# Performance work log

Hardware: AMD Instinct MI355X
Metric: run time of the kernel (lower is better)

## Reference

```python
import jax, jax.numpy as jnp
import numpy as np

B, T, D, E, H = 4, 2048, 1024, 4, 8
EPS = 1e-5


def _uniform(k, shape, bound):
    return jax.random.uniform(k, shape, jnp.float32, -bound, bound)


def setup_inputs() -> dict:
    key = jax.random.key(0)
    ks = jax.random.split(key, 12)
    wb = np.sqrt(6.0 / D) / np.sqrt(6.0)  # kaiming_uniform(a=sqrt5) bound ~ 1/sqrt(D)... keep simple
    wb = 1.0 / np.sqrt(D)
    return {
        "x": jax.random.normal(ks[0], (B, T, D), jnp.float32),
        "router_prob": jax.random.uniform(ks[1], (B, T, E), jnp.float32),
        "norm_w": jnp.ones((D,), jnp.float32),
        "norm_b": jnp.zeros((D,), jnp.float32),
        "q_w": _uniform(ks[2], (D, D), wb),
        "q_b": _uniform(ks[3], (D,), wb),
        "k_w": _uniform(ks[4], (D, D), wb),
        "k_b": _uniform(ks[5], (D,), wb),
        "v_w": _uniform(ks[6], (D, D), wb),
        "v_b": _uniform(ks[7], (D,), wb),
        "o_w": _uniform(ks[8], (D, D), wb),
        "o_b": _uniform(ks[9], (D,), wb),
    }


def _layernorm(x, w, b):
    mu = jnp.mean(x, axis=-1, keepdims=True)
    var = jnp.mean(jnp.square(x - mu), axis=-1, keepdims=True)
    return (x - mu) * jax.lax.rsqrt(var + EPS) * w + b


def reference(x, router_prob, norm_w, norm_b, q_w, q_b, k_w, k_b, v_w, v_b, o_w, o_b):
    e_cnt = router_prob.shape[2]
    b, t, d = x.shape
    n = t // e_cnt
    h = H
    scale = d ** (-0.5)  # note: original uses model_dim**-0.5, not head_dim

    qs, ks_, vs = [], [], []
    for e in range(e_cnt):
        xe = x[:, e * n:(e + 1) * n, :]
        xn = _layernorm(xe, norm_w, norm_b)
        m = d // (2 ** e)
        xm = xn[..., :m]  # [b, n, m] matryoshka slice
        # F.linear(xm, W[:, :m], bias): out = xm @ W[:, :m]^T + b -> [b, n, d]
        qs.append(jnp.einsum('bnm,dm->bnd', xm, q_w[:, :m]) + q_b)
        ks_.append(jnp.einsum('bnm,dm->bnd', xm, k_w[:, :m]) + k_b)
        vs.append(jnp.einsum('bnm,dm->bnd', xm, v_w[:, :m]) + v_b)
    q = jnp.concatenate(qs, axis=1)
    k = jnp.concatenate(ks_, axis=1)
    v = jnp.concatenate(vs, axis=1)

    dh = d // h
    q = q.reshape(b, t, h, dh).transpose(0, 2, 1, 3)  # b h t dh
    k = k.reshape(b, t, h, dh).transpose(0, 2, 1, 3)
    v = v.reshape(b, t, h, dh).transpose(0, 2, 1, 3)

    attn = jnp.einsum('bhqd,bhkd->bhqk', q, k) * scale
    attn = jax.nn.softmax(attn, axis=-1)  # dropout = identity in eval
    attn_out = jnp.einsum('bhqk,bhkd->bhqd', attn, v)
    attn_out = attn_out.transpose(0, 2, 1, 3).reshape(b, t, d)

    outs = []
    for e in range(e_cnt):
        sl = slice(e * n, (e + 1) * n)
        m = d // (2 ** e)
        xm = attn_out[:, sl, :m]
        out = jnp.einsum('bnm,om->bno', xm, o_w[:m, :m]) + o_b[:m]  # [b, n, m]
        pad = d - m
        if pad:
            out = jnp.pad(out, ((0, 0), (0, 0), (0, pad)))
        outs.append(out + x[:, sl, :])
    return jnp.concatenate(outs, axis=1)
```

## Files before the change

kernel.cpp:

```cpp
#include <hip/hip_runtime.h>
#include <hip/hip_bf16.h>

#define DEV static __device__ __forceinline__

typedef __attribute__((ext_vector_type(4))) float f32x4;
typedef __attribute__((ext_vector_type(8))) short s16x8;
typedef __attribute__((ext_vector_type(4))) unsigned int u32x4;

constexpr int Bn = 4, Tn = 2048, Dn = 1024, Hn = 8, DH = 128;
constexpr float EPSF = 1e-5f;
constexpr float QSCALE = 0.0450842200277801f;

DEV unsigned short f2bf(float f) {
    unsigned int u = __float_as_uint(f);
    u += 0x7FFF + ((u >> 16) & 1);
    return (unsigned short)(u >> 16);
}

DEV f32x4 mfma16(s16x8 a, s16x8 b, f32x4 c) {
    return __builtin_amdgcn_mfma_f32_16x16x32_bf16(a, b, c, 0, 0, 0);
}

DEV float ex2(float x) {
    float r;
    asm("v_exp_f32 %0, %1" : "=v"(r) : "v"(x));
    return r;
}

DEV unsigned int cvtpk(float lo, float hi) {
    unsigned int r;
    asm("v_cvt_pk_bf16_f32 %0, %1, %2" : "=v"(r) : "v"(lo), "v"(hi));
    return r;
}

typedef __attribute__((address_space(1))) const unsigned int GU32;
typedef __attribute__((address_space(3))) unsigned int LU32;
DEV void gload16(const void* g, void* l) {
    __builtin_amdgcn_global_load_lds((GU32*)g, (LU32*)l, 16, 0, 0);
}

__global__ void cvt_w_kernel(const float* __restrict__ qw, const float* __restrict__ kw,
                             const float* __restrict__ vw, const float* __restrict__ ow,
                             unsigned short* __restrict__ dst) {
    int idx = blockIdx.x * blockDim.x + threadIdx.x;
    const int total = 4 * Dn * Dn;
    for (; idx < total; idx += gridDim.x * blockDim.x) {
        int sel = idx >> 20;
        int off = idx & (Dn * Dn - 1);
        const float* src = sel == 0 ? qw : sel == 1 ? kw : sel == 2 ? vw : ow;
        dst[idx] = f2bf(src[off]);
    }
}

__global__ __launch_bounds__(256) void ln_kernel(const float* __restrict__ x,
                                                 const float* __restrict__ w,
                                                 const float* __restrict__ b,
                                                 unsigned short* __restrict__ xn) {
    int tok = blockIdx.x;
    int tid = threadIdx.x;
    const float* xp = x + (size_t)tok * Dn;
    float4 v = ((const float4*)xp)[tid];
    float s = v.x + v.y + v.z + v.w;
    float q = v.x * v.x + v.y * v.y + v.z * v.z + v.w * v.w;
    for (int off = 32; off; off >>= 1) {
        s += __shfl_xor(s, off);
        q += __shfl_xor(q, off);
    }
    __shared__ float red[8];
    __shared__ float stats[2];
    int wid = tid >> 6, lane = tid & 63;
    if (lane == 0) { red[wid] = s; red[4 + wid] = q; }
    __syncthreads();
    if (tid == 0) {
        float ts = red[0] + red[1] + red[2] + red[3];
        float tq = red[4] + red[5] + red[6] + red[7];
        float mu = ts / Dn;
        float var = tq / Dn - mu * mu;
        stats[0] = mu;
        stats[1] = rsqrtf(var + EPSF);
    }
    __syncthreads();
    float mu = stats[0], rs = stats[1];
    int c = tid * 4;
    ushort4 o;
    o.x = f2bf((v.x - mu) * rs * w[c + 0] + b[c + 0]);
    o.y = f2bf((v.y - mu) * rs * w[c + 1] + b[c + 1]);
    o.z = f2bf((v.z - mu) * rs * w[c + 2] + b[c + 2]);
    o.w = f2bf((v.w - mu) * rs * w[c + 3] + b[c + 3]);
    ((ushort4*)(xn + (size_t)tok * Dn))[tid] = o;
}

__global__ __launch_bounds__(256) void qkv_gemm(const unsigned short* __restrict__ xn,
                                                const unsigned short* __restrict__ wmat,
                                                const float* __restrict__ qb_,
                                                const float* __restrict__ kb_,
                                                const float* __restrict__ vb_,
                                                unsigned short* __restrict__ outq,
                                                unsigned short* __restrict__ outk,
                                                unsigned short* __restrict__ vt) {
    int rowbase = blockIdx.x * 128;
    int colbase = blockIdx.y * 128;
    int matid = blockIdx.z;
    const unsigned short* W = wmat + (size_t)matid * Dn * Dn;
    const float* bias = matid == 0 ? qb_ : matid == 1 ? kb_ : vb_;
    float oscale = matid == 0 ? QSCALE : 1.0f;
    int e = (rowbase & (Tn - 1)) >> 9;
    int m = Dn >> e;

    __shared__ alignas(16) unsigned short At[2][128 * 32];
    __shared__ alignas(16) unsigned short Bt[2][128 * 32];

    int tid = threadIdx.x;
    int lane = tid & 63, wv = tid >> 6;
    int wr = (wv >> 1) * 64, wc = (wv & 1) * 64;
    int fr = lane & 15, fg = lane >> 4;
    int srow = tid >> 2, scol = (tid & 3) * 8;
    const unsigned short* ga0 = xn + (size_t)(rowbase + srow) * Dn + scol;
    const unsigned short* ga1 = xn + (size_t)(rowbase + 64 + srow) * Dn + scol;
    const unsigned short* gb0 = W + (size_t)(colbase + srow) * Dn + scol;
    const unsigned short* gb1 = W + (size_t)(colbase + 64 + srow) * Dn + scol;

    f32x4 acc[4][4] = {};

    gload16(ga0, &At[0][tid * 8]);
    gload16(ga1, &At[0][2048 + tid * 8]);
    gload16(gb0, &Bt[0][tid * 8]);
    gload16(gb1, &Bt[0][2048 + tid * 8]);
    __syncthreads();

    for (int k = 0; k < m; k += 32) {
        int cur = (k >> 5) & 1;
        if (k + 32 < m) {
            int nb = cur ^ 1, kn = k + 32;
            gload16(ga0 + kn, &At[nb][tid * 8]);
            gload16(ga1 + kn, &At[nb][2048 + tid * 8]);
            gload16(gb0 + kn, &Bt[nb][tid * 8]);
            gload16(gb1 + kn, &Bt[nb][2048 + tid * 8]);
        }
        s16x8 a[4], b[4];
        #pragma unroll
        for (int i = 0; i < 4; i++) a[i] = *(const s16x8*)&At[cur][(wr + i * 16 + fr) * 32 + fg * 8];
        #pragma unroll
        for (int j = 0; j < 4; j++) b[j] = *(const s16x8*)&Bt[cur][(wc + j * 16 + fr) * 32 + fg * 8];
        #pragma unroll
        for (int i = 0; i < 4; i++)
            #pragma unroll
            for (int j = 0; j < 4; j++) acc[i][j] = mfma16(a[i], b[j], acc[i][j]);
        __syncthreads();
    }

    if (matid == 2) {
        #pragma unroll
        for (int i = 0; i < 4; i++)
            #pragma unroll
            for (int j = 0; j < 4; j++) {
                int col = colbase + wc + j * 16 + fr;
                float bv = bias[col];
                int row0 = rowbase + wr + i * 16 + fg * 4;
                int bb = row0 >> 11, tl = row0 & (Tn - 1);
                int w32 = tl & 31;
                int tlp = (tl & ~31) | (((w32 >> 2) & 3) * 8 + ((w32 >> 4) & 1) * 4);
                size_t base = (((size_t)bb * Hn + (col >> 7)) * DH + (col & (DH - 1))) * Tn + tlp;
                ushort4 o;
                o.x = f2bf(acc[i][j][0] + bv);
                o.y = f2bf(acc[i][j][1] + bv);
                o.z = f2bf(acc[i][j][2] + bv);
                o.w = f2bf(acc[i][j][3] + bv);
                *(ushort4*)&vt[base] = o;
            }
    } else {
        unsigned short* out = matid == 0 ? outq : outk;
        #pragma unroll
        for (int i = 0; i < 4; i++)
            #pragma unroll
            for (int j = 0; j < 4; j++) {
                int col = colbase + wc + j * 16 + fr;
                float bv = bias[col];
                #pragma unroll
                for (int r = 0; r < 4; r++) {
                    int row = rowbase + wr + i * 16 + fg * 4 + r;
                    out[(size_t)row * Dn + col] = f2bf((acc[i][j][r] + bv) * oscale);
                }
            }
    }
}

__global__ __launch_bounds__(256, 2) void attn_kernel(const unsigned short* __restrict__ Q,
                                                      const unsigned short* __restrict__ K,
                                                      const unsigned short* __restrict__ VT,
                                                      unsigned short* __restrict__ AO) {
    int f = blockIdx.x;
    int qi = f >> 5;
    int bh = f & 31;
    int b = bh >> 3, h = bh & 7;
    int qbase = qi * 128;
    int tid = threadIdx.x;
    int wv = tid >> 6, lane = tid & 63;
    int fr = lane & 15, fg = lane >> 4;

    __shared__ alignas(16) unsigned short Kt[2][64 * 128];
    __shared__ alignas(16) unsigned short Vt[2][128 * 64];

    s16x8 bq[2][4];
    #pragma unroll
    for (int hh = 0; hh < 2; hh++) {
        const size_t qr = ((size_t)b * Tn + qbase + wv * 32 + hh * 16 + fr) * Dn + h * DH;
        #pragma unroll
        for (int c = 0; c < 4; c++) bq[hh][c] = *(const s16x8*)&Q[qr + c * 32 + fg * 8];
    }

    f32x4 acc[2][8] = {};
    float m_run[2] = {-1e30f, -1e30f};
    float l_run[2] = {0.f, 0.f};

    const unsigned short* Kbase = K + (size_t)b * Tn * Dn + h * DH;
    const unsigned short* Vbase = VT + ((size_t)b * Hn + h) * DH * Tn;

    int k_row_lo = tid >> 4, k_chk = tid & 15;
    int v_row_lo = tid >> 3, v_chk = tid & 7;

    auto STAGE = [&](int t, int buf) {
        int kb = t * 64;
        #pragma unroll
        for (int p = 0; p < 4; p++) {
            int row = p * 16 + k_row_lo;
            int chunk = k_chk ^ (row & 7);
            gload16(Kbase + (size_t)(kb + row) * Dn + chunk * 8,
                    &Kt[buf][p * 2048 + tid * 8]);
        }
        #pragma unroll
        for (int p = 0; p < 4; p++) {
            int row = p * 32 + v_row_lo;
            int chunk = v_chk ^ (row & 7);
            gload16(Vbase + (size_t)row * Tn + kb + chunk * 8,
                    &Vt[buf][p * 2048 + tid * 8]);
        }
    };

    STAGE(0, 0);
    __syncthreads();

    for (int t = 0; t < Tn / 64; t++) {
        int cur = t & 1;
        if (t < Tn / 64 - 1) STAGE(t + 1, cur ^ 1);

        const unsigned short* KtC = &Kt[cur][0];
        const unsigned short* VtC = &Vt[cur][0];

        f32x4 s[2][4] = {};
        #pragma unroll
        for (int c = 0; c < 4; c++) {
            #pragma unroll
            for (int kt = 0; kt < 4; kt++) {
                s16x8 ak = *(const s16x8*)&KtC[(kt * 16 + fr) * 128 +
                                               (((c * 4 + fg) ^ (fr & 7)) * 8)];
                s[0][kt] = mfma16(ak, bq[0][c], s[0][kt]);
                s[1][kt] = mfma16(ak, bq[1][c], s[1][kt]);
            }
        }

        float mx[2];
        #pragma unroll
        for (int hh = 0; hh < 2; hh++) {
            float v = s[hh][0][0];
            #pragma unroll
            for (int kt = 0; kt < 4; kt++)
                #pragma unroll
                for (int r = 0; r < 4; r++) v = fmaxf(v, s[hh][kt][r]);
            v = fmaxf(v, __shfl_xor(v, 16));
            v = fmaxf(v, __shfl_xor(v, 32));
            mx[hh] = v;
        }

        if (!__all(mx[0] - m_run[0] <= 8.0f && mx[1] - m_run[1] <= 8.0f)) {
            #pragma unroll
            for (int hh = 0; hh < 2; hh++) {
                float mnew = fmaxf(m_run[hh], mx[hh]);
                float fsc = ex2(m_run[hh] - mnew);
                l_run[hh] *= fsc;
                float fw[4];
                #pragma unroll
                for (int r = 0; r < 4; r++) fw[r] = __shfl(fsc, fg * 4 + r);
                #pragma unroll
                for (int n = 0; n < 8; n++)
                    #pragma unroll
                    for (int r = 0; r < 4; r++) acc[hh][n][r] *= fw[r];
                m_run[hh] = mnew;
            }
        }

        s16x8 pa[2][2];
        #pragma unroll
        for (int hh = 0; hh < 2; hh++) {
            float p[16];
            float sum = 0.f;
            #pragma unroll
            for (int kt = 0; kt < 4; kt++)
                #pragma unroll
                for (int r = 0; r < 4; r++) {
                    float ev = ex2(s[hh][kt][r] - m_run[hh]);
                    p[kt * 4 + r] = ev;
                    sum += ev;
                }
            sum += __shfl_xor(sum, 16);
            sum += __shfl_xor(sum, 32);
            l_run[hh] += sum;
            #pragma unroll
            for (int ks = 0; ks < 2; ks++) {
                u32x4 pw;
                pw.x = cvtpk(p[ks * 8 + 0], p[ks * 8 + 1]);
                pw.y = cvtpk(p[ks * 8 + 2], p[ks * 8 + 3]);
                pw.z = cvtpk(p[ks * 8 + 4], p[ks * 8 + 5]);
                pw.w = cvtpk(p[ks * 8 + 6], p[ks * 8 + 7]);
                pa[hh][ks] = __builtin_bit_cast(s16x8, pw);
            }
        }

        #pragma unroll
        for (int ks = 0; ks < 2; ks++) {
            #pragma unroll
            for (int n = 0; n < 8; n++) {
                int row = n * 16 + fr;
                s16x8 bv = *(const s16x8*)&VtC[row * 64 +
                                               (((ks * 4 + fg) ^ (fr & 7)) * 8)];
                acc[0][n] = mfma16(pa[0][ks], bv, acc[0][n]);
                acc[1][n] = mfma16(pa[1][ks], bv, acc[1][n]);
            }
        }
        __syncthreads();
    }

    #pragma unroll
    for (int hh = 0; hh < 2; hh++) {
        float rl[4];
        #pragma unroll
        for (int r = 0; r < 4; r++) rl[r] = 1.0f / __shfl(l_run[hh], fg * 4 + r);
        size_t orow0 = ((size_t)b * Tn + qbase + wv * 32 + hh * 16) * Dn + h * DH;
        for (int n = 0; n < 8; n++)
            for (int r = 0; r < 4; r++) {
                float v = acc[hh][n][r] * rl[r];
                AO[orow0 + (size_t)(fg * 4 + r) * Dn + n * 16 + fr] = f2bf(v);
            }
    }
}

__global__ __launch_bounds__(256) void oproj_gemm(const unsigned short* __restrict__ A,
                                                  const unsigned short* __restrict__ W,
                                                  const float* __restrict__ bias,
                                                  const float* __restrict__ x,
                                                  float* __restrict__ out) {
    int rowbase = blockIdx.x * 128;
    int colbase = blockIdx.y * 128;
    int e = (rowbase & (Tn - 1)) >> 9;
    int m = Dn >> e;
    int tid = threadIdx.x;

    if (colbase >= m) {
        #pragma unroll
        for (int i = 0; i < 16; i++) {
            int idx = i * 256 + tid;
            int r = idx >> 5, c4 = (idx & 31) * 4;
            size_t g = (size_t)(rowbase + r) * Dn + colbase + c4;
            *(float4*)&out[g] = *(const float4*)&x[g];
        }
        return;
    }

    __shared__ alignas(16) unsigned short At[2][128 * 32];
    __shared__ alignas(16) unsigned short Bt[2][128 * 32];
    int lane = tid & 63, wv = tid >> 6;
    int wr = (wv >> 1) * 64, wc = (wv & 1) * 64;
    int fr = lane & 15, fg = lane >> 4;
    int srow = tid >> 2, scol = (tid & 3) * 8;
    const unsigned short* ga0 = A + (size_t)(rowbase + srow) * Dn + scol;
    const unsigned short* ga1 = A + (size_t)(rowbase + 64 + srow) * Dn + scol;
    const unsigned short* gb0 = W + (size_t)(colbase + srow) * Dn + scol;
    const unsigned short* gb1 = W + (size_t)(colbase + 64 + srow) * Dn + scol;

    f32x4 acc[4][4] = {};

    gload16(ga0, &At[0][tid * 8]);
    gload16(ga1, &At[0][2048 + tid * 8]);
    gload16(gb0, &Bt[0][tid * 8]);
    gload16(gb1, &Bt[0][2048 + tid * 8]);
    __syncthreads();

    for (int k = 0; k < m; k += 32) {
        int cur = (k >> 5) & 1;
        if (k + 32 < m) {
            int nb = cur ^ 1, kn = k + 32;
            gload16(ga0 + kn, &At[nb][tid * 8]);
            gload16(ga1 + kn, &At[nb][2048 + tid * 8]);
            gload16(gb0 + kn, &Bt[nb][tid * 8]);
            gload16(gb1 + kn, &Bt[nb][2048 + tid * 8]);
        }
        s16x8 a[4], b[4];
        #pragma unroll
        for (int i = 0; i < 4; i++) a[i] = *(const s16x8*)&At[cur][(wr + i * 16 + fr) * 32 + fg * 8];
        #pragma unroll
        for (int j = 0; j < 4; j++) b[j] = *(const s16x8*)&Bt[cur][(wc + j * 16 + fr) * 32 + fg * 8];
        #pragma unroll
        for (int i = 0; i < 4; i++)
            #pragma unroll
            for (int j = 0; j < 4; j++) acc[i][j] = mfma16(a[i], b[j], acc[i][j]);
        __syncthreads();
    }

    #pragma unroll
    for (int i = 0; i < 4; i++)
        #pragma unroll
        for (int j = 0; j < 4; j++) {
            int col = colbase + wc + j * 16 + fr;
            float bv = bias[col];
            #pragma unroll
            for (int r = 0; r < 4; r++) {
                int row = rowbase + wr + i * 16 + fg * 4 + r;
                size_t g = (size_t)row * Dn + col;
                out[g] = acc[i][j][r] + bv + x[g];
            }
        }
}

extern "C" void kernel_launch(void* const* d_in, const int* in_sizes, int n_in,
                              void* d_out, int out_size, void* d_ws, size_t ws_size,
                              hipStream_t stream) {
    const float* x   = (const float*)d_in[0];
    const float* nw  = (const float*)d_in[2];
    const float* nb  = (const float*)d_in[3];
    const float* qw  = (const float*)d_in[4];
    const float* qb_ = (const float*)d_in[5];
    const float* kw  = (const float*)d_in[6];
    const float* kb_ = (const float*)d_in[7];
    const float* vw  = (const float*)d_in[8];
    const float* vb_ = (const float*)d_in[9];
    const float* ow  = (const float*)d_in[10];
    const float* ob_ = (const float*)d_in[11];
    float* out = (float*)d_out;

    unsigned short* ws = (unsigned short*)d_ws;
    const size_t NTOK = (size_t)Bn * Tn;
    unsigned short* xn = ws;
    unsigned short* qd = xn + NTOK * Dn;
    unsigned short* kd = qd + NTOK * Dn;
    unsigned short* vt = kd + NTOK * Dn;
    unsigned short* ao = vt + NTOK * Dn;
    unsigned short* wb = ao + NTOK * Dn;

    hipLaunchKernelGGL(cvt_w_kernel, dim3(4096), dim3(256), 0, stream, qw, kw, vw, ow, wb);
    hipLaunchKernelGGL(ln_kernel, dim3(NTOK), dim3(256), 0, stream, x, nw, nb, xn);
    hipLaunchKernelGGL(qkv_gemm, dim3(64, 8, 3), dim3(256), 0, stream,
                       xn, wb, qb_, kb_, vb_, qd, kd, vt);
    hipLaunchKernelGGL(attn_kernel, dim3(512), dim3(256), 0, stream, qd, kd, vt, ao);
    hipLaunchKernelGGL(oproj_gemm, dim3(64, 8), dim3(256), 0, stream,
                       ao, wb + (size_t)3 * Dn * Dn, ob_, x, out);
}
```

Measured before the change: 188.5 us.

## Deepen GEMM prefetch to 4-stage ring and compute softmax denominator via MFMA

Both the QKV and output-projection GEMMs move from a double buffer to a 4-slot shared-memory ring that prefetches two tiles ahead. They use explicit vmcnt waits and a single barrier per step instead of a trailing __syncthreads, so global-load latency is hidden better. The attention kernel drops the per-tile row-sum reductions and their cross-lane shuffles. It instead accumulates the softmax denominator with an extra MFMA against a vector of ones, and raises wave priority around the MFMA blocks. This doubles GEMM shared-memory use and adds a ninth accumulator's worth of registers and MFMAs in attention, which could lower occupancy.

```diff
diff --git a/kernel.cpp b/kernel.cpp
--- a/kernel.cpp
+++ b/kernel.cpp
@@ -106,9 +106,10 @@
     float oscale = matid == 0 ? QSCALE : 1.0f;
     int e = (rowbase & (Tn - 1)) >> 9;
     int m = Dn >> e;
-
-    __shared__ alignas(16) unsigned short At[2][128 * 32];
-    __shared__ alignas(16) unsigned short Bt[2][128 * 32];
+    int nt = m >> 5;
+
+    __shared__ alignas(16) unsigned short At[4][128 * 32];
+    __shared__ alignas(16) unsigned short Bt[4][128 * 32];
 
     int tid = threadIdx.x;
     int lane = tid & 63, wv = tid >> 6;
@@ -122,21 +123,23 @@
 
     f32x4 acc[4][4] = {};
 
-    gload16(ga0, &At[0][tid * 8]);
-    gload16(ga1, &At[0][2048 + tid * 8]);
-    gload16(gb0, &Bt[0][tid * 8]);
-    gload16(gb1, &Bt[0][2048 + tid * 8]);
-    __syncthreads();
-
-    for (int k = 0; k < m; k += 32) {
-        int cur = (k >> 5) & 1;
-        if (k + 32 < m) {
-            int nb = cur ^ 1, kn = k + 32;
-            gload16(ga0 + kn, &At[nb][tid * 8]);
-            gload16(ga1 + kn, &At[nb][2048 + tid * 8]);
-            gload16(gb0 + kn, &Bt[nb][tid * 8]);
-            gload16(gb1 + kn, &Bt[nb][2048 + tid * 8]);
-        }
+    auto STAGE = [&](int tt) {
+        int buf = tt & 3, kk = tt * 32;
+        gload16(ga0 + kk, &At[buf][tid * 8]);
+        gload16(ga1 + kk, &At[buf][2048 + tid * 8]);
+        gload16(gb0 + kk, &Bt[buf][tid * 8]);
+        gload16(gb1 + kk, &Bt[buf][2048 + tid * 8]);
+    };
+
+    STAGE(0);
+    if (nt > 1) STAGE(1);
+
+    for (int t = 0; t < nt; t++) {
+        if (t + 1 < nt) { asm volatile("s_waitcnt vmcnt(4)" ::: "memory"); }
+        else            { asm volatile("s_waitcnt vmcnt(0)" ::: "memory"); }
+        __builtin_amdgcn_s_barrier();
+        if (t + 2 < nt) STAGE(t + 2);
+        int cur = t & 3;
         s16x8 a[4], b[4];
         #pragma unroll
         for (int i = 0; i < 4; i++) a[i] = *(const s16x8*)&At[cur][(wr + i * 16 + fr) * 32 + fg * 8];
@@ -146,7 +149,6 @@
         for (int i = 0; i < 4; i++)
             #pragma unroll
             for (int j = 0; j < 4; j++) acc[i][j] = mfma16(a[i], b[j], acc[i][j]);
-        __syncthreads();
     }
 
     if (matid == 2) {
@@ -209,9 +211,11 @@
         for (int c = 0; c < 4; c++) bq[hh][c] = *(const s16x8*)&Q[qr + c * 32 + fg * 8];
     }
 
-    f32x4 acc[2][8] = {};
+    const s16x8 ones = {(short)0x3F80, (short)0x3F80, (short)0x3F80, (short)0x3F80,
+                        (short)0x3F80, (short)0x3F80, (short)0x3F80, (short)0x3F80};
+
+    f32x4 acc[2][9] = {};
     float m_run[2] = {-1e30f, -1e30f};
-    float l_run[2] = {0.f, 0.f};
 
     const unsigned short* Kbase = K + (size_t)b * Tn * Dn + h * DH;
     const unsigned short* Vbase = VT + ((size_t)b * Hn + h) * DH * Tn;
@@ -248,6 +252,7 @@
         const unsigned short* VtC = &Vt[cur][0];
 
         f32x4 s[2][4] = {};
+        __builtin_amdgcn_s_setprio(1);
         #pragma unroll
         for (int c = 0; c < 4; c++) {
             #pragma unroll
@@ -258,6 +263,7 @@
                 s[1][kt] = mfma16(ak, bq[1][c], s[1][kt]);
             }
         }
+        __builtin_amdgcn_s_setprio(0);
 
         float mx[2];
         #pragma unroll
@@ -277,12 +283,11 @@
             for (int hh = 0; hh < 2; hh++) {
                 float mnew = fmaxf(m_run[hh], mx[hh]);
                 float fsc = ex2(m_run[hh] - mnew);
-                l_run[hh] *= fsc;
                 float fw[4];
                 #pragma unroll
                 for (int r = 0; r < 4; r++) fw[r] = __shfl(fsc, fg * 4 + r);
                 #pragma unroll
-                for (int n = 0; n < 8; n++)
+                for (int n = 0; n < 9; n++)
                     #pragma unroll
                     for (int r = 0; r < 4; r++) acc[hh][n][r] *= fw[r];
                 m_run[hh] = mnew;
@@ -293,18 +298,10 @@
         #pragma unroll
         for (int hh = 0; hh < 2; hh++) {
             float p[16];
-            float sum = 0.f;
             #pragma unroll
             for (int kt = 0; kt < 4; kt++)
                 #pragma unroll
-                for (int r = 0; r < 4; r++) {
-                    float ev = ex2(s[hh][kt][r] - m_run[hh]);
-                    p[kt * 4 + r] = ev;
-                    sum += ev;
-                }
-            sum += __shfl_xor(sum, 16);
-            sum += __shfl_xor(sum, 32);
-            l_run[hh] += sum;
+                for (int r = 0; r < 4; r++) p[kt * 4 + r] = ex2(s[hh][kt][r] - m_run[hh]);
             #pragma unroll
             for (int ks = 0; ks < 2; ks++) {
                 u32x4 pw;
@@ -316,6 +313,7 @@
             }
         }
 
+        __builtin_amdgcn_s_setprio(1);
         #pragma unroll
         for (int ks = 0; ks < 2; ks++) {
             #pragma unroll
@@ -326,7 +324,10 @@
                 acc[0][n] = mfma16(pa[0][ks], bv, acc[0][n]);
                 acc[1][n] = mfma16(pa[1][ks], bv, acc[1][n]);
             }
-        }
+            acc[0][8] = mfma16(pa[0][ks], ones, acc[0][8]);
+            acc[1][8] = mfma16(pa[1][ks], ones, acc[1][8]);
+        }
+        __builtin_amdgcn_s_setprio(0);
         __syncthreads();
     }
 
@@ -334,7 +335,7 @@
     for (int hh = 0; hh < 2; hh++) {
         float rl[4];
         #pragma unroll
-        for (int r = 0; r < 4; r++) rl[r] = 1.0f / __shfl(l_run[hh], fg * 4 + r);
+        for (int r = 0; r < 4; r++) rl[r] = 1.0f / acc[hh][8][r];
         size_t orow0 = ((size_t)b * Tn + qbase + wv * 32 + hh * 16) * Dn + h * DH;
         for (int n = 0; n < 8; n++)
             for (int r = 0; r < 4; r++) {
@@ -366,8 +367,8 @@
         return;
     }
 
-    __shared__ alignas(16) unsigned short At[2][128 * 32];
-    __shared__ alignas(16) unsigned short Bt[2][128 * 32];
+    __shared__ alignas(16) unsigned short At[4][128 * 32];
+    __shared__ alignas(16) unsigned short Bt[4][128 * 32];
     int lane = tid & 63, wv = tid >> 6;
     int wr = (wv >> 1) * 64, wc = (wv & 1) * 64;
     int fr = lane & 15, fg = lane >> 4;
@@ -376,24 +377,27 @@
     const unsigned short* ga1 = A + (size_t)(rowbase + 64 + srow) * Dn + scol;
     const unsigned short* gb0 = W + (size_t)(colbase + srow) * Dn + scol;
     const unsigned short* gb1 = W + (size_t)(colbase + 64 + srow) * Dn + scol;
+    int nt = m >> 5;
 
     f32x4 acc[4][4] = {};
 
-    gload16(ga0, &At[0][tid * 8]);
-    gload16(ga1, &At[0][2048 + tid * 8]);
-    gload16(gb0, &Bt[0][tid * 8]);
-    gload16(gb1, &Bt[0][2048 + tid * 8]);
-    __syncthreads();
-
-    for (int k = 0; k < m; k += 32) {
-        int cur = (k >> 5) & 1;
-        if (k + 32 < m) {
-            int nb = cur ^ 1, kn = k + 32;
-            gload16(ga0 + kn, &At[nb][tid * 8]);
-            gload16(ga1 + kn, &At[nb][2048 + tid * 8]);
-            gload16(gb0 + kn, &Bt[nb][tid * 8]);
-            gload16(gb1 + kn, &Bt[nb][2048 + tid * 8]);
-        }
+    auto STAGE = [&](int tt) {
+        int buf = tt & 3, kk = tt * 32;
+        gload16(ga0 + kk, &At[buf][tid * 8]);
+        gload16(ga1 + kk, &At[buf][2048 + tid * 8]);
+        gload16(gb0 + kk, &Bt[buf][tid * 8]);
+        gload16(gb1 + kk, &Bt[buf][2048 + tid * 8]);
+    };
+
+    STAGE(0);
+    if (nt > 1) STAGE(1);
+
+    for (int t = 0; t < nt; t++) {
+        if (t + 1 < nt) { asm volatile("s_waitcnt vmcnt(4)" ::: "memory"); }
+        else            { asm volatile("s_waitcnt vmcnt(0)" ::: "memory"); }
+        __builtin_amdgcn_s_barrier();
+        if (t + 2 < nt) STAGE(t + 2);
+        int cur = t & 3;
         s16x8 a[4], b[4];
         #pragma unroll
         for (int i = 0; i < 4; i++) a[i] = *(const s16x8*)&At[cur][(wr + i * 16 + fr) * 32 + fg * 8];
@@ -403,7 +407,6 @@
         for (int i = 0; i < 4; i++)
             #pragma unroll
             for (int j = 0; j < 4; j++) acc[i][j] = mfma16(a[i], b[j], acc[i][j]);
-        __syncthreads();
     }
 
     #pragma unroll
```

New measurement: 187.6 us. About the same (-0.5%).
